# Optimization experiments

Hardware: AMD Instinct MI355X
Metric: run time of the kernel (lower is better)

The kernel has to match this reference:

```python
import jax, jax.numpy as jnp
import numpy as np

ALPHA = 0.5
BETA = 0.5
THRESHOLD = 0.5


def connected_components(fg):
    """4-connected component labeling (scipy.ndimage.label default structure)
    via iterative min-label propagation. fg: bool [B,H,W]. Returns int32 labels,
    0 = background; foreground labels are arbitrary unique ids per component."""
    B, H, W = fg.shape
    BIG = jnp.int32(H * W + 2)
    idx = (jnp.arange(H * W, dtype=jnp.int32) + 1).reshape(1, H, W)
    labels0 = jnp.where(fg, jnp.broadcast_to(idx, (B, H, W)), 0)

    def nbr_min(l):
        lf = jnp.where(fg, l, BIG)
        up = jnp.concatenate([jnp.full((B, 1, W), BIG, jnp.int32), lf[:, :-1]], 1)
        dn = jnp.concatenate([lf[:, 1:], jnp.full((B, 1, W), BIG, jnp.int32)], 1)
        lt = jnp.concatenate([jnp.full((B, H, 1), BIG, jnp.int32), lf[:, :, :-1]], 2)
        rt = jnp.concatenate([lf[:, :, 1:], jnp.full((B, H, 1), BIG, jnp.int32)], 2)
        m = jnp.minimum(jnp.minimum(up, dn), jnp.minimum(lt, rt))
        return jnp.where(fg, jnp.minimum(lf, m), 0)

    def cond(carry):
        return carry[1]

    def body(carry):
        l, _ = carry
        nl = nbr_min(l)
        return nl, jnp.any(nl != l)

    labels, _ = jax.lax.while_loop(cond, body, (labels0, jnp.bool_(True)))
    return labels


def detect_critical(labels_a, fg_b):
    """Mark every connected component of `labels_a` that contains at least one
    voxel not covered by foreground of the other segmentation (`fg_b`), i.e.
    components touched by a mismatch -> topologically critical. Per-sample."""
    H, W = labels_a.shape
    mismatch = ((labels_a > 0) & (~fg_b)).astype(jnp.int32)
    cnt = jax.ops.segment_sum(mismatch.ravel(), labels_a.ravel(), num_segments=H * W + 1)
    return ((cnt[labels_a] > 0) & (labels_a > 0)).astype(jnp.float32)


def get_critical_masks(pred_bin, target_bin):
    # pred_bin/target_bin: bool [B,H,W]
    pred_lbl = connected_components(pred_bin)
    tgt_lbl = connected_components(target_bin)
    neg = jax.vmap(detect_critical)(tgt_lbl, pred_bin)   # critical comps of target (false-neg)
    pos = jax.vmap(detect_critical)(pred_lbl, target_bin)  # critical comps of pred (false-pos)
    return BETA * neg + (1.0 - BETA) * pos  # [B,H,W]


def setup_inputs() -> dict:
    key = jax.random.key(0)
    k1, k2 = jax.random.split(key)
    B, C, H, W = 8, 1, 512, 512
    preds = jax.random.normal(k1, (B, C, H, W), dtype=jnp.float32)
    targets = (jax.random.uniform(k2, (B, C, H, W)) > 0.5).astype(jnp.float32)
    return {"preds": preds, "targets": targets}


def reference(preds, targets):
    # BCEWithLogitsLoss(reduction='none', pos_weight=1)
    loss = -(targets * jax.nn.log_sigmoid(preds)
             + (1.0 - targets) * jax.nn.log_sigmoid(-preds))  # [B,1,H,W]
    pred_bin = preds[:, 0] > THRESHOLD          # binarize(preds[:,0,...])
    target_bin = targets[:, 0] != 0.0           # scipy.label treats nonzero as fg
    masks = get_critical_masks(pred_bin, target_bin)  # [B,H,W]
    blended = (1.0 - ALPHA) * loss + ALPHA * masks[:, None] * loss
    return blended.mean()
```

## Files before the change

### kernel.cpp

```cpp
#include <hip/hip_runtime.h>
#include <math.h>

#define BATCH 8
#define HH 512
#define WW 512
#define IMG (HH * WW)
#define NTOT (BATCH * IMG)
#define TROWS 4
#define TS (TROWS * WW)
#define NTILES (NTOT / TS)
#define BPF (BATCH * (HH / TROWS - 1) * WW)
#define THRESH 0.5f
#define NBLK (NTOT / 256)


__device__ __forceinline__ int findroot_g(const int* p, int x) {
    int px;
    while ((px = p[x]) != x) x = px;
    return x;
}

__device__ __forceinline__ void unite_g(int* p, int a, int b) {
    bool done = false;
    do {
        a = findroot_g(p, a);
        b = findroot_g(p, b);
        if (a > b) {
            int old = atomicMin(&p[a], b);
            done = (old == a);
            a = old;
        } else if (b > a) {
            int old = atomicMin(&p[b], a);
            done = (old == b);
            b = old;
        } else {
            done = true;
        }
    } while (!done);
}

__device__ __forceinline__ int findroot_s(const int* p, int x) {
    int px;
    while ((px = p[x]) != x) x = px;
    return x;
}

__device__ __forceinline__ void unite_s(int* p, int a, int b) {
    bool done = false;
    do {
        a = findroot_s(p, a);
        b = findroot_s(p, b);
        if (a > b) {
            int old = atomicMin(&p[a], b);
            done = (old == a);
            a = old;
        } else if (b > a) {
            int old = atomicMin(&p[b], a);
            done = (old == b);
            b = old;
        } else {
            done = true;
        }
    } while (!done);
}


__global__ void __launch_bounds__(256) k_local(const float* __restrict__ preds,
                                               const float* __restrict__ targets,
                                               int* __restrict__ pP, int* __restrict__ pT,
                                               unsigned long long* __restrict__ flags64) {
    __shared__ int lp[TS];
    int bid = blockIdx.x;
    int field = bid >> 10;
    int tb = bid & (NTILES - 1);
    const float* __restrict__ src = field ? targets : preds;
    int* __restrict__ gp = field ? pT : pP;
    const int base = tb * TS;

    flags64[bid * 256 + threadIdx.x] = 0ull;

    const float4* __restrict__ src4 = (const float4*)(src + base);
    for (int i = threadIdx.x; i < TS / 4; i += 256) {
        float4 v = src4[i];
        int l = 4 * i;
        if (field) {
            lp[l]     = (v.x != 0.0f) ? l     : -1;
            lp[l + 1] = (v.y != 0.0f) ? l + 1 : -1;
            lp[l + 2] = (v.z != 0.0f) ? l + 2 : -1;
            lp[l + 3] = (v.w != 0.0f) ? l + 3 : -1;
        } else {
            lp[l]     = (v.x > THRESH) ? l     : -1;
            lp[l + 1] = (v.y > THRESH) ? l + 1 : -1;
            lp[l + 2] = (v.z > THRESH) ? l + 2 : -1;
            lp[l + 3] = (v.w > THRESH) ? l + 3 : -1;
        }
    }
    __syncthreads();

    const int lane = threadIdx.x & 63;

    for (int l = threadIdx.x; l < TS; l += 256) {
        int wbase = l & ~63;
        bool fg = lp[l] >= 0;
        unsigned long long m = __ballot(fg);
        int col0 = wbase & (WW - 1);
        bool left0 = (col0 != 0) && (lp[wbase - 1] >= 0);
        unsigned long long starts = m & ~(m << 1);
        if (left0) starts &= ~1ull;
        unsigned long long below = starts & (~0ull >> (63 - lane));
        if (fg) {
            int dst = below ? (wbase + (63 - __clzll(below)))
                            : (wbase - 1);
            lp[l] = dst;
        }
    }
    __syncthreads();

    for (int l = threadIdx.x; l < TS - WW; l += 256) {
        if (lp[l] < 0 || lp[l + WW] < 0) continue;
        int col = l & (WW - 1);
        if (col != 0 && lp[l - 1] >= 0 && lp[l + WW - 1] >= 0) continue;
        unite_s(lp, l, l + WW);
    }
    __syncthreads();

    for (int l = threadIdx.x; l < TS; l += 256) {
        int out = -1;
        if (lp[l] >= 0) out = base + findroot_s(lp, l);
        gp[base + l] = out;
    }
}


__global__ void k_border(int* __restrict__ pP, int* __restrict__ pT) {
    int id = blockIdx.x * blockDim.x + threadIdx.x;
    if (id >= 2 * BPF) return;
    int field = (id >= BPF) ? 1 : 0;
    int r = id - field * BPF;
    int* p = field ? pT : pP;
    const int perimg = (HH / TROWS - 1) * WW;
    int img = r / perimg;
    int rem = r - img * perimg;
    int b = rem >> 9;
    int c = rem & (WW - 1);
    int row = b * TROWS + (TROWS - 1);
    int n = img * IMG + row * WW + c;
    int ra = p[n];
    int rb = p[n + WW];
    if (ra >= 0 && rb >= 0) unite_g(p, ra, rb);
}


__global__ void k_flatmark(int* __restrict__ pP, int* __restrict__ pT,
                           unsigned char* __restrict__ flagP8,
                           unsigned char* __restrict__ flagT8) {
    int n = blockIdx.x * blockDim.x + threadIdx.x;
    if (n >= NTOT) return;
    int a = pP[n];
    int b = pT[n];
    bool fp = a >= 0;
    bool ft = b >= 0;
    if (fp) {
        int r = a, pr;
        while ((pr = pP[r]) != r) r = pr;
        if (a != r) pP[n] = r;
        if (!ft) flagP8[r] = 1;
    }
    if (ft) {
        int r = b, pr;
        while ((pr = pT[r]) != r) r = pr;
        if (b != r) pT[n] = r;
        if (!fp) flagT8[r] = 1;
    }
}


__device__ __forceinline__ float softplusf(float z) {
    return fmaxf(z, 0.0f) + log1pf(expf(-fabsf(z)));
}

__device__ __forceinline__ float block_reduce_sum(float v, float* smem4) {
    for (int off = 32; off > 0; off >>= 1) v += __shfl_down(v, off, 64);
    int lane = threadIdx.x & 63, wid = threadIdx.x >> 6;
    if (lane == 0) smem4[wid] = v;
    __syncthreads();
    return smem4[0] + smem4[1] + smem4[2] + smem4[3];
}

__global__ void k_gather(const float* __restrict__ preds, const float* __restrict__ targets,
                         const int* __restrict__ pP, const int* __restrict__ pT,
                         const unsigned char* __restrict__ flagP8,
                         const unsigned char* __restrict__ flagT8,
                         float* __restrict__ partial) {
    int n = blockIdx.x * blockDim.x + threadIdx.x;
    float contrib = 0.0f;
    if (n < NTOT) {
        float x = preds[n];
        float t = targets[n];
        float loss = t * softplusf(-x) + (1.0f - t) * softplusf(x);
        int a = pP[n];
        int b = pT[n];
        float m = 0.0f;
        if (b >= 0 && flagT8[b]) m += 0.5f;
        if (a >= 0 && flagP8[a]) m += 0.5f;
        contrib = (0.5f + 0.5f * m) * loss;
    }
    __shared__ float smem4[4];
    float s = block_reduce_sum(contrib, smem4);
    if (threadIdx.x == 0) partial[blockIdx.x] = s;
}

__global__ void k_final(const float* __restrict__ partial, float* __restrict__ out) {
    float s = 0.0f;
    for (int i = threadIdx.x; i < NBLK; i += 256) s += partial[i];
    __shared__ float smem4[4];
    float tot = block_reduce_sum(s, smem4);
    if (threadIdx.x == 0) out[0] = tot / (float)NTOT;
}


extern "C" void kernel_launch(void* const* d_in, const int* in_sizes, int n_in,
                              void* d_out, int out_size, void* d_ws, size_t ws_size,
                              hipStream_t stream) {
    const float* preds = (const float*)d_in[0];
    const float* targets = (const float*)d_in[1];

    int* pP = (int*)d_ws;
    int* pT = pP + NTOT;
    unsigned char* flagP8 = (unsigned char*)(pT + NTOT);
    unsigned char* flagT8 = flagP8 + NTOT;
    float* partial = (float*)(flagT8 + NTOT);
    float* out = (float*)d_out;

    const int block = 256;

    k_local<<<2 * NTILES, block, 0, stream>>>(preds, targets, pP, pT,
                                              (unsigned long long*)flagP8);
    k_border<<<(2 * BPF + block - 1) / block, block, 0, stream>>>(pP, pT);
    k_flatmark<<<NBLK, block, 0, stream>>>(pP, pT, flagP8, flagT8);
    k_gather<<<NBLK, block, 0, stream>>>(preds, targets, pP, pT, flagP8, flagT8, partial);
    k_final<<<1, 256, 0, stream>>>(partial, out);
}
```

Before: 76.29 us.

## Compress only local roots via a bitmap instead of flattening every pixel

k_local now writes a per-64-pixel ballot bitmap of which pixels are tile-local roots. A new k_rootcomp kernel walks only those set bits and points each local root straight at its global root. k_mark and k_gather then reach the global label through a two-level lookup p[p[n]], instead of running a full find-root for every pixel. This is meant to remove the per-pixel pointer chasing of the old k_flatmark, at the cost of an extra kernel launch and extra dependent gathers in the mark and gather passes.

```diff
diff --git a/kernel.cpp b/kernel.cpp
--- a/kernel.cpp
+++ b/kernel.cpp
@@ -12,6 +12,7 @@
 #define BPF (BATCH * (HH / TROWS - 1) * WW)
 #define THRESH 0.5f
 #define NBLK (NTOT / 256)
+#define WPF (NTOT / 64)
 
 
 __device__ __forceinline__ int findroot_g(const int* p, int x) {
@@ -68,13 +69,16 @@
 __global__ void __launch_bounds__(256) k_local(const float* __restrict__ preds,
                                                const float* __restrict__ targets,
                                                int* __restrict__ pP, int* __restrict__ pT,
-                                               unsigned long long* __restrict__ flags64) {
+                                               unsigned long long* __restrict__ flags64,
+                                               unsigned long long* __restrict__ bmP,
+                                               unsigned long long* __restrict__ bmT) {
     __shared__ int lp[TS];
     int bid = blockIdx.x;
     int field = bid >> 10;
     int tb = bid & (NTILES - 1);
     const float* __restrict__ src = field ? targets : preds;
     int* __restrict__ gp = field ? pT : pP;
+    unsigned long long* __restrict__ bm = field ? bmT : bmP;
     const int base = tb * TS;
 
     flags64[bid * 256 + threadIdx.x] = 0ull;
@@ -128,6 +132,8 @@
         int out = -1;
         if (lp[l] >= 0) out = base + findroot_s(lp, l);
         gp[base + l] = out;
+        unsigned long long isroot = __ballot(out == base + l);
+        if (lane == 0) bm[(base + (l & ~63)) >> 6] = isroot;
     }
 }
 
@@ -151,27 +157,36 @@
 }
 
 
-__global__ void k_flatmark(int* __restrict__ pP, int* __restrict__ pT,
-                           unsigned char* __restrict__ flagP8,
-                           unsigned char* __restrict__ flagT8) {
+__global__ void __launch_bounds__(256) k_rootcomp(const unsigned long long* __restrict__ bm,
+                                                  int* __restrict__ pP, int* __restrict__ pT) {
+    int id = blockIdx.x * blockDim.x + threadIdx.x;
+    int wi = id >> 2;
+    if (wi >= 2 * WPF) return;
+    unsigned long long w = bm[wi];
+    unsigned int bits = (unsigned int)((w >> ((id & 3) * 16)) & 0xFFFFull);
+    if (!bits) return;
+    int field = wi >= WPF;
+    int* p = field ? pT : pP;
+    int basepx = (wi - field * WPF) * 64 + (id & 3) * 16;
+    while (bits) {
+        int b = __ffs(bits) - 1;
+        bits &= bits - 1;
+        int x = basepx + b;
+        int r = x, pr;
+        while ((pr = p[r]) != r) r = pr;
+        if (p[x] != r) p[x] = r;
+    }
+}
+
+
+__global__ void k_mark(const int* __restrict__ pP, const int* __restrict__ pT,
+                       unsigned char* __restrict__ flagP8,
+                       unsigned char* __restrict__ flagT8) {
     int n = blockIdx.x * blockDim.x + threadIdx.x;
-    if (n >= NTOT) return;
     int a = pP[n];
     int b = pT[n];
-    bool fp = a >= 0;
-    bool ft = b >= 0;
-    if (fp) {
-        int r = a, pr;
-        while ((pr = pP[r]) != r) r = pr;
-        if (a != r) pP[n] = r;
-        if (!ft) flagP8[r] = 1;
-    }
-    if (ft) {
-        int r = b, pr;
-        while ((pr = pT[r]) != r) r = pr;
-        if (b != r) pT[n] = r;
-        if (!fp) flagT8[r] = 1;
-    }
+    if (a >= 0 && b < 0) flagP8[pP[a]] = 1;
+    if (b >= 0 && a < 0) flagT8[pT[b]] = 1;
 }
 
 
@@ -193,18 +208,16 @@
                          const unsigned char* __restrict__ flagT8,
                          float* __restrict__ partial) {
     int n = blockIdx.x * blockDim.x + threadIdx.x;
-    float contrib = 0.0f;
-    if (n < NTOT) {
-        float x = preds[n];
-        float t = targets[n];
-        float loss = t * softplusf(-x) + (1.0f - t) * softplusf(x);
-        int a = pP[n];
-        int b = pT[n];
-        float m = 0.0f;
-        if (b >= 0 && flagT8[b]) m += 0.5f;
-        if (a >= 0 && flagP8[a]) m += 0.5f;
-        contrib = (0.5f + 0.5f * m) * loss;
-    }
+    float x = preds[n];
+    float t = targets[n];
+    float loss = t * softplusf(-x) + (1.0f - t) * softplusf(x);
+    int a = pP[n];
+    int b = pT[n];
+    float m = 0.0f;
+    if (b >= 0 && flagT8[pT[b]]) m += 0.5f;
+    if (a >= 0 && flagP8[pP[a]]) m += 0.5f;
+    float contrib = (0.5f + 0.5f * m) * loss;
+
     __shared__ float smem4[4];
     float s = block_reduce_sum(contrib, smem4);
     if (threadIdx.x == 0) partial[blockIdx.x] = s;
@@ -229,15 +242,18 @@
     int* pT = pP + NTOT;
     unsigned char* flagP8 = (unsigned char*)(pT + NTOT);
     unsigned char* flagT8 = flagP8 + NTOT;
-    float* partial = (float*)(flagT8 + NTOT);
+    unsigned long long* bmP = (unsigned long long*)(flagT8 + NTOT);
+    unsigned long long* bmT = bmP + WPF;
+    float* partial = (float*)(bmT + WPF);
     float* out = (float*)d_out;
 
     const int block = 256;
 
     k_local<<<2 * NTILES, block, 0, stream>>>(preds, targets, pP, pT,
-                                              (unsigned long long*)flagP8);
+                                              (unsigned long long*)flagP8, bmP, bmT);
     k_border<<<(2 * BPF + block - 1) / block, block, 0, stream>>>(pP, pT);
-    k_flatmark<<<NBLK, block, 0, stream>>>(pP, pT, flagP8, flagT8);
+    k_rootcomp<<<(2 * WPF * 4 + block - 1) / block, block, 0, stream>>>(bmP, pP, pT);
+    k_mark<<<NBLK, block, 0, stream>>>(pP, pT, flagP8, flagT8);
     k_gather<<<NBLK, block, 0, stream>>>(preds, targets, pP, pT, flagP8, flagT8, partial);
     k_final<<<1, 256, 0, stream>>>(partial, out);
 }
```

After: 88.89 us. 1.17x slower.
